# Optimization experiments

Hardware: AMD Instinct MI355X
Metric: run time of the kernel (lower is better)

## Reference

```python
import jax, jax.numpy as jnp
import numpy as np

D_MODEL = 2048
N_HEADS = 16
D_K = D_MODEL // N_HEADS
NB_FEAT = 8  # ceil(ln(2048))
BLOCK_H = 1
BLOCK_W = 1
EPS = 1e-6


def setup_inputs() -> dict:
    key = jax.random.key(0)
    ks = jax.random.split(key, 8)
    B, S = 2, 4096
    q = jax.random.normal(ks[0], (B, S, D_MODEL), dtype=jnp.float32)
    k = jax.random.normal(ks[1], (B, S, D_MODEL), dtype=jnp.float32)
    v = jax.random.normal(ks[2], (B, S, D_MODEL), dtype=jnp.float32)
    # torch Linear weights [out, in]
    w_q = jax.random.normal(ks[3], (D_MODEL, D_MODEL), dtype=jnp.float32) / np.sqrt(D_MODEL)
    w_k = jax.random.normal(ks[4], (D_MODEL, D_MODEL), dtype=jnp.float32) / np.sqrt(D_MODEL)
    w_v = jax.random.normal(ks[5], (D_MODEL, D_MODEL), dtype=jnp.float32) / np.sqrt(D_MODEL)
    w_o = jax.random.normal(ks[6], (D_MODEL, D_MODEL), dtype=jnp.float32) / np.sqrt(D_MODEL)
    omega = jax.random.normal(ks[7], (NB_FEAT, D_K), dtype=jnp.float32) / np.sqrt(D_K)
    return {"q": q, "k": k, "v": v, "w_q": w_q, "w_k": w_k, "w_v": w_v, "w_o": w_o, "omega": omega}


def _kernel(x):
    # kernel_type == 'exp'
    return jnp.exp(-0.5 * x * x)


def reference(q, k, v, w_q, w_k, w_v, w_o, omega):
    B, Sq, D = q.shape
    Sk = k.shape[1]
    # projections (torch Linear: x @ W.T), split heads -> [B, S, H, d_k]
    qh = (q @ w_q.T).reshape(B, Sq, N_HEADS, D_K)
    kh = (k @ w_k.T).reshape(B, Sk, N_HEADS, D_K)
    vh = (v @ w_v.T).reshape(B, Sk, N_HEADS, D_K)
    # random-feature maps -> [B, S, H, nb]
    q_prime = _kernel(jnp.einsum('bshd,nd->bshn', qh, omega))
    k_prime = _kernel(jnp.einsum('bshd,nd->bshn', kh, omega))
    q_prime = q_prime / (q_prime.sum(-1, keepdims=True) + EPS)
    k_prime = k_prime / (k_prime.sum(-1, keepdims=True) + EPS)
    # causal prefix sums along sequence
    K_cum = jnp.cumsum(k_prime, axis=1)                                   # [B,S,H,nb]
    KV_cum = jnp.cumsum(k_prime[..., None] * vh[..., None, :], axis=1)    # [B,S,H,nb,d_k]
    # blockwise causal key selection
    q_idx = jnp.arange(Sq)
    key_idx = jnp.minimum((q_idx // BLOCK_H + 1) * BLOCK_W - 1, Sk - 1)   # [Sq]
    K_sel = K_cum[:, key_idx]    # [B,Sq,H,nb]
    KV_sel = KV_cum[:, key_idx]  # [B,Sq,H,nb,d_k]
    numerator = jnp.einsum('bshn,bshnd->bshd', q_prime, KV_sel)
    denominator = jnp.sum(q_prime * K_sel, axis=-1, keepdims=True)
    out = numerator / (denominator + EPS)
    out = out.reshape(B, Sq, D)
    return out @ w_o.T
```

## Files before the change

### kernel.cpp

```cpp
#include <hip/hip_runtime.h>
#include <hip/hip_bf16.h>
#include <cstdint>

#define B_SZ 2
#define S_LEN 4096
#define R_TOT 8192
#define DM 2048
#define NH 16
#define DK 128
#define NFEAT 8
#define CHUNK 128
#define NCHUNK 32
#define KSPL 256
#define NSPL 8
#define EPSF 1e-6f

typedef short bf16x8_t __attribute__((ext_vector_type(8)));
typedef float f32x4_t __attribute__((ext_vector_type(4)));

__device__ __forceinline__ ushort f2bf(float f) {
  uint32_t u = __float_as_uint(f);
  u += 0x7FFF + ((u >> 16) & 1);
  return (ushort)(u >> 16);
}
__device__ __forceinline__ float bf2f(ushort u) {
  return __uint_as_float(((uint32_t)u) << 16);
}

__global__ __launch_bounds__(256) void prep_kernel(const float* __restrict__ w_v,
                                                   const float* __restrict__ w_o,
                                                   const float* __restrict__ w_q,
                                                   const float* __restrict__ w_k,
                                                   const float* __restrict__ omega,
                                                   ushort* __restrict__ wvb,
                                                   ushort* __restrict__ wob,
                                                   ushort* __restrict__ oqb,
                                                   ushort* __restrict__ okb) {
  const int bid = blockIdx.x;
  if (bid < 8192) {
    const float* src = (bid >= 4096) ? w_o : w_v;
    ushort* dst = (bid >= 4096) ? wob : wvb;
    const int i = (bid & 4095) * 256 + threadIdx.x;
    float4 f = reinterpret_cast<const float4*>(src)[i];
    ushort4 o;
    o.x = f2bf(f.x); o.y = f2bf(f.y); o.z = f2bf(f.z); o.w = f2bf(f.w);
    reinterpret_cast<ushort4*>(dst)[i] = o;
  } else {
    __shared__ float som[NFEAT * DK];
    const int fb = bid - 8192;
    const int z = fb >> 7, h = (fb >> 3) & 15, jb = fb & 7;
    const float* W = z ? w_k : w_q;
    ushort* O = z ? okb : oqb;
    const int j = jb * 256 + threadIdx.x;
    for (int i = threadIdx.x; i < NFEAT * DK; i += 256) som[i] = omega[i];
    __syncthreads();
    float acc[NFEAT] = {0.f, 0.f, 0.f, 0.f, 0.f, 0.f, 0.f, 0.f};
    for (int d = 0; d < DK; d++) {
      const float w = W[(size_t)(h * DK + d) * DM + j];
#pragma unroll
      for (int n = 0; n < NFEAT; n++) acc[n] += w * som[n * DK + d];
    }
#pragma unroll
    for (int n = 0; n < NFEAT; n++) O[(size_t)(h * NFEAT + n) * DM + j] = f2bf(acc[n]);
  }
}

#define MFMA_BLK(mb, A0_, A1_, A2_, A3_, B0_, B1_, B2_, B3_)                                  \
  acc[mb + 0][0] = __builtin_amdgcn_mfma_f32_16x16x32_bf16(A0_, B0_, acc[mb + 0][0], 0, 0, 0); \
  acc[mb + 1][0] = __builtin_amdgcn_mfma_f32_16x16x32_bf16(A1_, B0_, acc[mb + 1][0], 0, 0, 0); \
  acc[mb + 2][0] = __builtin_amdgcn_mfma_f32_16x16x32_bf16(A2_, B0_, acc[mb + 2][0], 0, 0, 0); \
  acc[mb + 3][0] = __builtin_amdgcn_mfma_f32_16x16x32_bf16(A3_, B0_, acc[mb + 3][0], 0, 0, 0); \
  acc[mb + 0][1] = __builtin_amdgcn_mfma_f32_16x16x32_bf16(A0_, B1_, acc[mb + 0][1], 0, 0, 0); \
  acc[mb + 1][1] = __builtin_amdgcn_mfma_f32_16x16x32_bf16(A1_, B1_, acc[mb + 1][1], 0, 0, 0); \
  acc[mb + 2][1] = __builtin_amdgcn_mfma_f32_16x16x32_bf16(A2_, B1_, acc[mb + 2][1], 0, 0, 0); \
  acc[mb + 3][1] = __builtin_amdgcn_mfma_f32_16x16x32_bf16(A3_, B1_, acc[mb + 3][1], 0, 0, 0); \
  acc[mb + 0][2] = __builtin_amdgcn_mfma_f32_16x16x32_bf16(A0_, B2_, acc[mb + 0][2], 0, 0, 0); \
  acc[mb + 1][2] = __builtin_amdgcn_mfma_f32_16x16x32_bf16(A1_, B2_, acc[mb + 1][2], 0, 0, 0); \
  acc[mb + 2][2] = __builtin_amdgcn_mfma_f32_16x16x32_bf16(A2_, B2_, acc[mb + 2][2], 0, 0, 0); \
  acc[mb + 3][2] = __builtin_amdgcn_mfma_f32_16x16x32_bf16(A3_, B2_, acc[mb + 3][2], 0, 0, 0); \
  acc[mb + 0][3] = __builtin_amdgcn_mfma_f32_16x16x32_bf16(A0_, B3_, acc[mb + 0][3], 0, 0, 0); \
  acc[mb + 1][3] = __builtin_amdgcn_mfma_f32_16x16x32_bf16(A1_, B3_, acc[mb + 1][3], 0, 0, 0); \
  acc[mb + 2][3] = __builtin_amdgcn_mfma_f32_16x16x32_bf16(A2_, B3_, acc[mb + 2][3], 0, 0, 0); \
  acc[mb + 3][3] = __builtin_amdgcn_mfma_f32_16x16x32_bf16(A3_, B3_, acc[mb + 3][3], 0, 0, 0);

template<int BF16OUT>
__global__ __launch_bounds__(512, 1) void gemm256(const ushort* __restrict__ A,
                                                  const ushort* __restrict__ Bm,
                                                  void* __restrict__ Cv,
                                                  int M, int N, int K) {
  __shared__ ushort lds[8 * 8192];
  const int tid = threadIdx.x;
  const int wave = tid >> 6, lane = tid & 63;
  const int wm = wave >> 2, wn = wave & 3;
  const int NKT = K >> 6;

  const int nb = N >> 8;
  const int cpx = gridDim.x >> 3;
  const int swz = (blockIdx.x & 7) * cpx + (blockIdx.x >> 3);
  const int bx = swz % nb, by = swz / nb;
  const int m0 = by * 256, n0 = bx * 256;

  auto stage = [&](int bufi, int ab, int kh, int kt, const ushort* G, int r0) {
    ushort* Lr = lds + (((bufi << 1) | ab) << 1 | kh) * 8192;
#pragma unroll
    for (int j = 0; j < 2; j++) {
      const int c = j * 512 + wave * 64 + lane;
      const int row = c >> 2, slot = c & 3;
      const int ss = slot ^ ((row >> 1) & 3);
      const ushort* g = G + (size_t)(r0 + row) * K + kt * 64 + kh * 32 + ss * 8;
      __builtin_amdgcn_global_load_lds(
          (const __attribute__((address_space(1))) void*)g,
          (__attribute__((address_space(3))) void*)(Lr + (j * 512 + wave * 64) * 8), 16, 0, 0);
    }
  };
  auto rdA = [&](int bufi, int kh, int m) -> bf16x8_t {
    const int row = wm * 128 + m * 16 + (lane & 15);
    const int slot = (lane >> 4) ^ ((row >> 1) & 3);
    return *reinterpret_cast<const bf16x8_t*>(lds + ((bufi << 2) | kh) * 8192 + row * 32 + slot * 8);
  };
  auto rdB = [&](int bufi, int kh, int nf) -> bf16x8_t {
    const int row = wn * 64 + nf * 16 + (lane & 15);
    const int slot = (lane >> 4) ^ ((row >> 1) & 3);
    return *reinterpret_cast<const bf16x8_t*>(lds + (((bufi << 1) | 1) << 1 | kh) * 8192 + row * 32 + slot * 8);
  };

  f32x4_t acc[8][4];
#pragma unroll
  for (int m = 0; m < 8; m++)
#pragma unroll
    for (int nf = 0; nf < 4; nf++) acc[m][nf] = (f32x4_t){0.f, 0.f, 0.f, 0.f};

  stage(0, 0, 0, 0, A, m0);  stage(0, 1, 0, 0, Bm, n0);
  stage(0, 0, 1, 0, A, m0);  stage(0, 1, 1, 0, Bm, n0);
  stage(1, 0, 0, 1, A, m0);  stage(1, 1, 0, 1, Bm, n0);
  asm volatile("s_waitcnt vmcnt(8)" ::: "memory");
  __builtin_amdgcn_s_barrier();
  __builtin_amdgcn_sched_barrier(0);

  bf16x8_t pA0 = rdA(0, 0, 0), pA1 = rdA(0, 0, 1), pA2 = rdA(0, 0, 2), pA3 = rdA(0, 0, 3);
  bf16x8_t B00 = rdB(0, 0, 0), B01 = rdB(0, 0, 1), B02 = rdB(0, 0, 2), B03 = rdB(0, 0, 3);
  bf16x8_t qA0, qA1, qA2, qA3, B10, B11, B12, B13;

  for (int t = 0; t < NKT; t++) {
    const int buf = t & 1;
    const int t1 = (t + 1 < NKT) ? t + 1 : NKT - 1;
    const int t2 = (t + 2 < NKT) ? t + 2 : NKT - 1;

    qA0 = rdA(buf, 0, 4); qA1 = rdA(buf, 0, 5); qA2 = rdA(buf, 0, 6); qA3 = rdA(buf, 0, 7);
    stage(buf ^ 1, 0, 1, t1, A, m0);
    __builtin_amdgcn_s_setprio(1);
    MFMA_BLK(0, pA0, pA1, pA2, pA3, B00, B01, B02, B03)
    __builtin_amdgcn_s_setprio(0);
    asm volatile("s_waitcnt vmcnt(6)" ::: "memory");
    __builtin_amdgcn_s_barrier();
    __builtin_amdgcn_sched_barrier(0);

    pA0 = rdA(buf, 1, 0); pA1 = rdA(buf, 1, 1); pA2 = rdA(buf, 1, 2); pA3 = rdA(buf, 1, 3);
    B10 = rdB(buf, 1, 0); B11 = rdB(buf, 1, 1); B12 = rdB(buf, 1, 2); B13 = rdB(buf, 1, 3);
    stage(buf ^ 1, 1, 1, t1, Bm, n0);
    __builtin_amdgcn_s_setprio(1);
    MFMA_BLK(4, qA0, qA1, qA2, qA3, B00, B01, B02, B03)
    __builtin_amdgcn_s_setprio(0);
    __builtin_amdgcn_s_barrier();
    __builtin_amdgcn_sched_barrier(0);

    qA0 = rdA(buf, 1, 4); qA1 = rdA(buf, 1, 5); qA2 = rdA(buf, 1, 6); qA3 = rdA(buf, 1, 7);
    stage(buf, 0, 0, t2, A, m0);
    __builtin_amdgcn_s_setprio(1);
    MFMA_BLK(0, pA0, pA1, pA2, pA3, B10, B11, B12, B13)
    __builtin_amdgcn_s_setprio(0);
    asm volatile("s_waitcnt vmcnt(6)" ::: "memory");
    __builtin_amdgcn_s_barrier();
    __builtin_amdgcn_sched_barrier(0);

    pA0 = rdA(buf ^ 1, 0, 0); pA1 = rdA(buf ^ 1, 0, 1); pA2 = rdA(buf ^ 1, 0, 2); pA3 = rdA(buf ^ 1, 0, 3);
    B00 = rdB(buf ^ 1, 0, 0); B01 = rdB(buf ^ 1, 0, 1); B02 = rdB(buf ^ 1, 0, 2); B03 = rdB(buf ^ 1, 0, 3);
    stage(buf, 1, 0, t2, Bm, n0);
    __builtin_amdgcn_s_setprio(1);
    MFMA_BLK(4, qA0, qA1, qA2, qA3, B10, B11, B12, B13)
    __builtin_amdgcn_s_setprio(0);
    __builtin_amdgcn_s_barrier();
    __builtin_amdgcn_sched_barrier(0);
  }
  asm volatile("s_waitcnt vmcnt(0)" ::: "memory");

#pragma unroll
  for (int m = 0; m < 8; m++) {
    const int rb = m0 + wm * 128 + m * 16 + (lane >> 4) * 4;
#pragma unroll
    for (int nf = 0; nf < 4; nf++) {
      const int col = n0 + wn * 64 + nf * 16 + (lane & 15);
#pragma unroll
      for (int r = 0; r < 4; r++) {
        const float val = acc[m][nf][r];
        if (BF16OUT)
          ((ushort*)Cv)[(size_t)(rb + r) * N + col] = f2bf(val);
        else
          ((float*)Cv)[(size_t)(rb + r) * N + col] = val;
      }
    }
  }
}

__global__ __launch_bounds__(256) void gemm_thin2(const float* __restrict__ qin,
                                                  const float* __restrict__ kin,
                                                  const float* __restrict__ vin,
                                                  const ushort* __restrict__ oqb,
                                                  const ushort* __restrict__ okb,
                                                  ushort* __restrict__ P,
                                                  ushort* __restrict__ xb) {
  __shared__ ushort lds_a[128 * 32];
  __shared__ ushort lds_b[128 * 32];
  const int which = blockIdx.z;
  const float* A = which ? kin : qin;
  const ushort* Bm = which ? okb : oqb;
  const int t = threadIdx.x;
  const int wave = t >> 6, lane = t & 63;
  const int spl = blockIdx.x;
  const int m0 = blockIdx.y * 128;
  const int kb = spl * KSPL;
  const int wm = wave >> 1, wn = wave & 1;
  const int NIT = KSPL / 32;

  const int fbid = (blockIdx.z * gridDim.y + blockIdx.y) * gridDim.x + blockIdx.x;
  const float4* v4 = reinterpret_cast<const float4*>(vin);
  ushort4* x4 = reinterpret_cast<ushort4*>(xb);
  const int vbase = fbid * 4096;

  f32x4_t acc[4][4];
#pragma unroll
  for (int i = 0; i < 4; i++)
#pragma unroll
    for (int j = 0; j < 4; j++) acc[i][j] = (f32x4_t){0.f, 0.f, 0.f, 0.f};

  const int srow = lane >> 2;
  const int skoff = (lane & 3) * 8;
  const int ar0 = t >> 2, ar1 = 64 + (t >> 2), aslot = t & 3;

  const float4* ga0 = reinterpret_cast<const float4*>(A + (size_t)(m0 + ar0) * DM + kb + aslot * 8);
  const float4* ga1 = reinterpret_cast<const float4*>(A + (size_t)(m0 + ar1) * DM + kb + aslot * 8);
  float4 aP0 = ga0[0], aP1 = ga0[1], aP2 = ga1[0], aP3 = ga1[1];
  float4 va = v4[vbase + t], vb = v4[vbase + 256 + t];

  for (int it = 0; it < NIT; ++it) {
    const int k0 = kb + it * 32;
    {
      ushort4 oa, ob;
      oa.x = f2bf(va.x); oa.y = f2bf(va.y); oa.z = f2bf(va.z); oa.w = f2bf(va.w);
      ob.x = f2bf(vb.x); ob.y = f2bf(vb.y); ob.z = f2bf(vb.z); ob.w = f2bf(vb.w);
      x4[vbase + it * 512 + t] = oa;
      x4[vbase + it * 512 + 256 + t] = ob;
    }
    {
      union { ushort u[8]; bf16x8_t v; } p0, p1;
      p0.u[0] = f2bf(aP0.x); p0.u[1] = f2bf(aP0.y); p0.u[2] = f2bf(aP0.z); p0.u[3] = f2bf(aP0.w);
      p0.u[4] = f2bf(aP1.x); p0.u[5] = f2bf(aP1.y); p0.u[6] = f2bf(aP1.z); p0.u[7] = f2bf(aP1.w);
      p1.u[0] = f2bf(aP2.x); p1.u[1] = f2bf(aP2.y); p1.u[2] = f2bf(aP2.z); p1.u[3] = f2bf(aP2.w);
      p1.u[4] = f2bf(aP3.x); p1.u[5] = f2bf(aP3.y); p1.u[6] = f2bf(aP3.z); p1.u[7] = f2bf(aP3.w);
      *reinterpret_cast<bf16x8_t*>(lds_a + ar0 * 32 + aslot * 8) = p0.v;
      *reinterpret_cast<bf16x8_t*>(lds_a + ar1 * 32 + aslot * 8) = p1.v;
    }
#pragma unroll
    for (int i = 0; i < 2; i++) {
      const int rgrp = i * 4 + wave;
      const int row = rgrp * 16 + srow;
      const ushort* gb = Bm + (size_t)row * DM + (k0 + skoff);
      __builtin_amdgcn_global_load_lds(
          (const __attribute__((address_space(1))) void*)gb,
          (__attribute__((address_space(3))) void*)(lds_b + rgrp * 512), 16, 0, 0);
    }
    __builtin_amdgcn_sched_barrier(0);
    if (it + 1 < NIT) {
      const float4* gn0 = reinterpret_cast<const float4*>(A + (size_t)(m0 + ar0) * DM + (k0 + 32) + aslot * 8);
      const float4* gn1 = reinterpret_cast<const float4*>(A + (size_t)(m0 + ar1) * DM + (k0 + 32) + aslot * 8);
      aP0 = gn0[0]; aP1 = gn0[1]; aP2 = gn1[0]; aP3 = gn1[1];
      va = v4[vbase + (it + 1) * 512 + t];
      vb = v4[vbase + (it + 1) * 512 + 256 + t];
      asm volatile("s_waitcnt vmcnt(6) lgkmcnt(0)" ::: "memory");
    } else {
      asm volatile("s_waitcnt vmcnt(0) lgkmcnt(0)" ::: "memory");
    }
    __builtin_amdgcn_s_barrier();
    __builtin_amdgcn_sched_barrier(0);
    bf16x8_t af[4], bfr[4];
#pragma unroll
    for (int i = 0; i < 4; i++) {
      af[i]  = *reinterpret_cast<const bf16x8_t*>(
          lds_a + (wm * 64 + i * 16 + (lane & 15)) * 32 + (lane >> 4) * 8);
      bfr[i] = *reinterpret_cast<const bf16x8_t*>(
          lds_b + (wn * 64 + i * 16 + (lane & 15)) * 32 + (lane >> 4) * 8);
    }
#pragma unroll
    for (int i = 0; i < 4; i++)
#pragma unroll
      for (int j = 0; j < 4; j++)
        acc[i][j] = __builtin_amdgcn_mfma_f32_16x16x32_bf16(af[i], bfr[j], acc[i][j], 0, 0, 0);
    __builtin_amdgcn_s_barrier();
    __builtin_amdgcn_sched_barrier(0);
  }

  ushort* Pp = P + (size_t)which * ((size_t)NSPL * R_TOT * 128) + (size_t)spl * ((size_t)R_TOT * 128);
#pragma unroll
  for (int i = 0; i < 4; i++) {
    const int rb = m0 + wm * 64 + i * 16 + (lane >> 4) * 4;
#pragma unroll
    for (int j = 0; j < 4; j++) {
      const int col = wn * 64 + j * 16 + (lane & 15);
#pragma unroll
      for (int r = 0; r < 4; r++)
        Pp[(size_t)(rb + r) * 128 + col] = f2bf(acc[i][j][r]);
    }
  }
}

__global__ __launch_bounds__(256) void feat2x2(const ushort* __restrict__ P,
                                               float* __restrict__ qf,
                                               float* __restrict__ kf) {
  const int which = blockIdx.y;
  const ushort* Pb = P + (size_t)which * ((size_t)NSPL * R_TOT * 128);
  float* F = which ? kf : qf;
  const int g = blockIdx.x * 256 + threadIdx.x;
  const int row = g >> 4, h = g & 15;
  float x[8] = {0.f, 0.f, 0.f, 0.f, 0.f, 0.f, 0.f, 0.f};
#pragma unroll
  for (int s = 0; s < NSPL; s++) {
    const bf16x8_t u = *reinterpret_cast<const bf16x8_t*>(
        Pb + (size_t)s * ((size_t)R_TOT * 128) + (size_t)row * 128 + h * NFEAT);
#pragma unroll
    for (int n = 0; n < 8; n++) x[n] += bf2f((ushort)u[n]);
  }
  float f[8], sum = 0.f;
#pragma unroll
  for (int n = 0; n < 8; n++) { f[n] = __expf(-0.5f * x[n] * x[n]); sum += f[n]; }
  const float inv = 1.f / (sum + EPSF);
  const int b = row >> 12, sidx = row & 4095;
  float* out = F + ((size_t)(h * 2 + b) * 4096 + sidx) * 8;
  float4 o0 = {f[0] * inv, f[1] * inv, f[2] * inv, f[3] * inv};
  float4 o1 = {f[4] * inv, f[5] * inv, f[6] * inv, f[7] * inv};
  reinterpret_cast<float4*>(out)[0] = o0;
  reinterpret_cast<float4*>(out)[1] = o1;
}

__global__ __launch_bounds__(128) void chunk_sum_kernel(const float* __restrict__ KF,
                                                        const ushort* __restrict__ VH,
                                                        float* __restrict__ CKV,
                                                        float* __restrict__ CK) {
  const int cid = blockIdx.x;
  const int c = cid & 31, bh = cid >> 5, b = bh >> 4, h = bh & 15;
  const int d = threadIdx.x;
  __shared__ float s_kf[CHUNK * 8];
  const size_t fbase = ((size_t)(h * 2 + b) * 4096 + (size_t)c * CHUNK) * 8;
  {
    float4 a0 = *reinterpret_cast<const float4*>(KF + fbase + d * 8);
    float4 a1 = *reinterpret_cast<const float4*>(KF + fbase + d * 8 + 4);
    *reinterpret_cast<float4*>(s_kf + d * 8) = a0;
    *reinterpret_cast<float4*>(s_kf + d * 8 + 4) = a1;
  }
  __syncthreads();
  float kv[8] = {0, 0, 0, 0, 0, 0, 0, 0};
  float ks = 0.f;
  const ushort* vp = VH + ((size_t)b * S_LEN + (size_t)c * CHUNK) * DM + h * DK + d;
  for (int s = 0; s < CHUNK; s++) {
    const float v = bf2f(vp[(size_t)s * DM]);
#pragma unroll
    for (int n = 0; n < 8; n++) kv[n] += s_kf[s * 8 + n] * v;
    ks += s_kf[s * 8 + (d & 7)];
  }
#pragma unroll
  for (int n = 0; n < 8; n++) CKV[((size_t)cid * 8 + n) * 128 + d] = kv[n];
  if (d < 8) CK[cid * 8 + d] = ks;
}

__global__ __launch_bounds__(128) void chunk_scan2(float* __restrict__ CKV,
                                                   float* __restrict__ CK) {
  const int bh = blockIdx.x >> 3, n = blockIdx.x & 7;
  const int d = threadIdx.x;
  float v[NCHUNK];
#pragma unroll
  for (int c = 0; c < NCHUNK; c++)
    v[c] = CKV[((size_t)(bh * NCHUNK + c) * 8 + n) * 128 + d];
  float run = 0.f;
#pragma unroll
  for (int c = 0; c < NCHUNK; c++) {
    const float tv = v[c];
    CKV[((size_t)(bh * NCHUNK + c) * 8 + n) * 128 + d] = run;
    run += tv;
  }
  if (d < 32) {
    const int i = (bh * NCHUNK + d) * 8 + n;
    const float orig = CK[i];
    float inc = orig;
#pragma unroll
    for (int off = 1; off < 32; off <<= 1) {
      const float o = __shfl_up(inc, off, 32);
      if (d >= off) inc += o;
    }
    CK[i] = inc - orig;
  }
}

__global__ __launch_bounds__(128) void attn_scan_kernel(const float* __restrict__ QF,
                                                        const float* __restrict__ KF,
                                                        const ushort* __restrict__ VH,
                                                        const float* __restrict__ CKV,
                                                        const float* __restrict__ CK,
                                                        ushort* __restrict__ AO) {
  const int cid = blockIdx.x;
  const int c = cid & 31, bh = cid >> 5, b = bh >> 4, h = bh & 15;
  const int d = threadIdx.x;
  __shared__ float s_qf[CHUNK * 8];
  __shared__ float s_kf[CHUNK * 8];
  const size_t fbase = ((size_t)(h * 2 + b) * 4096 + (size_t)c * CHUNK) * 8;
  {
    float4 a0 = *reinterpret_cast<const float4*>(QF + fbase + d * 8);
    float4 a1 = *reinterpret_cast<const float4*>(QF + fbase + d * 8 + 4);
    float4 b0 = *reinterpret_cast<const float4*>(KF + fbase + d * 8);
    float4 b1 = *reinterpret_cast<const float4*>(KF + fbase + d * 8 + 4);
    *reinterpret_cast<float4*>(s_qf + d * 8) = a0;
    *reinterpret_cast<float4*>(s_qf + d * 8 + 4) = a1;
    *reinterpret_cast<float4*>(s_kf + d * 8) = b0;
    *reinterpret_cast<float4*>(s_kf + d * 8 + 4) = b1;
  }
  float kv[8], krun[8];
#pragma unroll
  for (int n = 0; n < 8; n++) kv[n] = CKV[((size_t)cid * 8 + n) * 128 + d];
#pragma unroll
  for (int n = 0; n < 8; n++) krun[n] = CK[cid * 8 + n];
  __syncthreads();
  const size_t row0 = (size_t)b * S_LEN + (size_t)c * CHUNK;
  const ushort* vp = VH + row0 * DM + h * DK + d;
  ushort* op = AO + row0 * DM + h * DK + d;
  for (int s = 0; s < CHUNK; s++) {
    const float v = bf2f(vp[(size_t)s * DM]);
    float num = 0.f, den = 0.f;
#pragma unroll
    for (int n = 0; n < 8; n++) {
      const float kf = s_kf[s * 8 + n];
      kv[n] += kf * v;
      krun[n] += kf;
      const float qf = s_qf[s * 8 + n];
      num += qf * kv[n];
      den += qf * krun[n];
    }
    op[(size_t)s * DM] = f2bf(num / (den + EPSF));
  }
}

extern "C" void kernel_launch(void* const* d_in, const int* in_sizes, int n_in,
                              void* d_out, int out_size, void* d_ws, size_t ws_size,
                              hipStream_t stream) {
  const float* q     = (const float*)d_in[0];
  const float* k     = (const float*)d_in[1];
  const float* v     = (const float*)d_in[2];
  const float* w_q   = (const float*)d_in[3];
  const float* w_k   = (const float*)d_in[4];
  const float* w_v   = (const float*)d_in[5];
  const float* w_o   = (const float*)d_in[6];
  const float* omega = (const float*)d_in[7];

  char* ws = (char*)d_ws;
  const size_t DD2 = (size_t)DM * DM * 2;
  const size_t OD2 = (size_t)NH * NFEAT * DM * 2;
  const size_t RD2 = (size_t)R_TOT * DM * 2;
  const size_t X4  = (size_t)R_TOT * NH * NFEAT * 4;

  ushort* wvb = (ushort*)(ws);
  ushort* wob = (ushort*)(ws + DD2);
  ushort* oqb = (ushort*)(ws + 2 * DD2);
  ushort* okb = (ushort*)(ws + 2 * DD2 + OD2);
  ushort* xb  = (ushort*)(ws + 2 * DD2 + 2 * OD2);
  ushort* vhb = (ushort*)(ws + 2 * DD2 + 2 * OD2 + RD2);
  ushort* xp  = (ushort*)(ws + 2 * DD2 + 2 * OD2 + RD2);
  float*  qf  = (float*) (ws + 2 * DD2 + 2 * OD2 + 2 * RD2);
  float*  kf  = (float*) (ws + 2 * DD2 + 2 * OD2 + 2 * RD2 + X4);
  float*  ckv = (float*) (ws + 2 * DD2 + 2 * OD2 + 2 * RD2 + 2 * X4);
  float*  ck  = (float*) (ws + 2 * DD2 + 2 * OD2 + 2 * RD2 + 3 * X4);
  ushort* ao  = xb;

  prep_kernel<<<dim3(8448), 256, 0, stream>>>(w_v, w_o, w_q, w_k, omega,
                                              wvb, wob, oqb, okb);

  gemm_thin2<<<dim3(NSPL, R_TOT / 128, 2), 256, 0, stream>>>(q, k, v, oqb, okb, xp, xb);
  feat2x2<<<dim3(R_TOT * NH / 256, 2), 256, 0, stream>>>(xp, qf, kf);

  gemm256<1><<<dim3((R_TOT / 256) * (DM / 256)), 512, 0, stream>>>(xb, wvb, (void*)vhb, R_TOT, DM, DM);

  chunk_sum_kernel<<<dim3(B_SZ * NH * NCHUNK), 128, 0, stream>>>(kf, vhb, ckv, ck);
  chunk_scan2<<<dim3(B_SZ * NH * 8), 128, 0, stream>>>(ckv, ck);
  attn_scan_kernel<<<dim3(B_SZ * NH * NCHUNK), 128, 0, stream>>>(qf, kf, vhb, ckv, ck, ao);

  gemm256<0><<<dim3((R_TOT / 256) * (DM / 256)), 512, 0, stream>>>(ao, wob, d_out, R_TOT, DM, DM);
}
```

Before: 293.1 us.

## Rewrite thin feature projection GEMM as LDS-free per-wave MFMA kernel

Replaces the LDS-staged, double-barriered thin GEMM that projects q/k onto the folded omega weights with a kernel in which each wave owns 16 rows. A fragments are loaded straight from global memory and converted to bf16 in registers, and B fragments are read directly from global or L2. The grid doubles to 64-row blocks, and the fused fp32-to-bf16 conversion of v is reorganised into a straight unrolled loop. This removes LDS traffic and barriers and adds parallelism. In exchange, B is reloaded from cache by every wave, and the global access pattern is less coalesced.

```diff
diff --git a/kernel.cpp b/kernel.cpp
--- a/kernel.cpp
+++ b/kernel.cpp
@@ -202,114 +202,65 @@
   }
 }
 
-__global__ __launch_bounds__(256) void gemm_thin2(const float* __restrict__ qin,
-                                                  const float* __restrict__ kin,
-                                                  const float* __restrict__ vin,
-                                                  const ushort* __restrict__ oqb,
-                                                  const ushort* __restrict__ okb,
-                                                  ushort* __restrict__ P,
-                                                  ushort* __restrict__ xb) {
-  __shared__ ushort lds_a[128 * 32];
-  __shared__ ushort lds_b[128 * 32];
+__global__ __launch_bounds__(256) void featproj(const float* __restrict__ qin,
+                                                const float* __restrict__ kin,
+                                                const float* __restrict__ vin,
+                                                const ushort* __restrict__ oqb,
+                                                const ushort* __restrict__ okb,
+                                                ushort* __restrict__ P,
+                                                ushort* __restrict__ xb) {
   const int which = blockIdx.z;
   const float* A = which ? kin : qin;
   const ushort* Bm = which ? okb : oqb;
   const int t = threadIdx.x;
   const int wave = t >> 6, lane = t & 63;
+  const int l15 = lane & 15, lk = lane >> 4;
   const int spl = blockIdx.x;
-  const int m0 = blockIdx.y * 128;
+  const int row0 = blockIdx.y * 64 + wave * 16;
   const int kb = spl * KSPL;
-  const int wm = wave >> 1, wn = wave & 1;
-  const int NIT = KSPL / 32;
 
   const int fbid = (blockIdx.z * gridDim.y + blockIdx.y) * gridDim.x + blockIdx.x;
   const float4* v4 = reinterpret_cast<const float4*>(vin);
   ushort4* x4 = reinterpret_cast<ushort4*>(xb);
-  const int vbase = fbid * 4096;
-
-  f32x4_t acc[4][4];
-#pragma unroll
-  for (int i = 0; i < 4; i++)
-#pragma unroll
-    for (int j = 0; j < 4; j++) acc[i][j] = (f32x4_t){0.f, 0.f, 0.f, 0.f};
-
-  const int srow = lane >> 2;
-  const int skoff = (lane & 3) * 8;
-  const int ar0 = t >> 2, ar1 = 64 + (t >> 2), aslot = t & 3;
-
-  const float4* ga0 = reinterpret_cast<const float4*>(A + (size_t)(m0 + ar0) * DM + kb + aslot * 8);
-  const float4* ga1 = reinterpret_cast<const float4*>(A + (size_t)(m0 + ar1) * DM + kb + aslot * 8);
-  float4 aP0 = ga0[0], aP1 = ga0[1], aP2 = ga1[0], aP3 = ga1[1];
-  float4 va = v4[vbase + t], vb = v4[vbase + 256 + t];
-
-  for (int it = 0; it < NIT; ++it) {
-    const int k0 = kb + it * 32;
-    {
-      ushort4 oa, ob;
-      oa.x = f2bf(va.x); oa.y = f2bf(va.y); oa.z = f2bf(va.z); oa.w = f2bf(va.w);
-      ob.x = f2bf(vb.x); ob.y = f2bf(vb.y); ob.z = f2bf(vb.z); ob.w = f2bf(vb.w);
-      x4[vbase + it * 512 + t] = oa;
-      x4[vbase + it * 512 + 256 + t] = ob;
-    }
-    {
-      union { ushort u[8]; bf16x8_t v; } p0, p1;
-      p0.u[0] = f2bf(aP0.x); p0.u[1] = f2bf(aP0.y); p0.u[2] = f2bf(aP0.z); p0.u[3] = f2bf(aP0.w);
-      p0.u[4] = f2bf(aP1.x); p0.u[5] = f2bf(aP1.y); p0.u[6] = f2bf(aP1.z); p0.u[7] = f2bf(aP1.w);
-      p1.u[0] = f2bf(aP2.x); p1.u[1] = f2bf(aP2.y); p1.u[2] = f2bf(aP2.z); p1.u[3] = f2bf(aP2.w);
-      p1.u[4] = f2bf(aP3.x); p1.u[5] = f2bf(aP3.y); p1.u[6] = f2bf(aP3.z); p1.u[7] = f2bf(aP3.w);
-      *reinterpret_cast<bf16x8_t*>(lds_a + ar0 * 32 + aslot * 8) = p0.v;
-      *reinterpret_cast<bf16x8_t*>(lds_a + ar1 * 32 + aslot * 8) = p1.v;
-    }
-#pragma unroll
-    for (int i = 0; i < 2; i++) {
-      const int rgrp = i * 4 + wave;
-      const int row = rgrp * 16 + srow;
-      const ushort* gb = Bm + (size_t)row * DM + (k0 + skoff);
-      __builtin_amdgcn_global_load_lds(
-          (const __attribute__((address_space(1))) void*)gb,
-          (__attribute__((address_space(3))) void*)(lds_b + rgrp * 512), 16, 0, 0);
-    }
-    __builtin_amdgcn_sched_barrier(0);
-    if (it + 1 < NIT) {
-      const float4* gn0 = reinterpret_cast<const float4*>(A + (size_t)(m0 + ar0) * DM + (k0 + 32) + aslot * 8);
-      const float4* gn1 = reinterpret_cast<const float4*>(A + (size_t)(m0 + ar1) * DM + (k0 + 32) + aslot * 8);
-      aP0 = gn0[0]; aP1 = gn0[1]; aP2 = gn1[0]; aP3 = gn1[1];
-      va = v4[vbase + (it + 1) * 512 + t];
-      vb = v4[vbase + (it + 1) * 512 + 256 + t];
-      asm volatile("s_waitcnt vmcnt(6) lgkmcnt(0)" ::: "memory");
-    } else {
-      asm volatile("s_waitcnt vmcnt(0) lgkmcnt(0)" ::: "memory");
-    }
-    __builtin_amdgcn_s_barrier();
-    __builtin_amdgcn_sched_barrier(0);
-    bf16x8_t af[4], bfr[4];
-#pragma unroll
-    for (int i = 0; i < 4; i++) {
-      af[i]  = *reinterpret_cast<const bf16x8_t*>(
-          lds_a + (wm * 64 + i * 16 + (lane & 15)) * 32 + (lane >> 4) * 8);
-      bfr[i] = *reinterpret_cast<const bf16x8_t*>(
-          lds_b + (wn * 64 + i * 16 + (lane & 15)) * 32 + (lane >> 4) * 8);
-    }
-#pragma unroll
-    for (int i = 0; i < 4; i++)
-#pragma unroll
-      for (int j = 0; j < 4; j++)
-        acc[i][j] = __builtin_amdgcn_mfma_f32_16x16x32_bf16(af[i], bfr[j], acc[i][j], 0, 0, 0);
-    __builtin_amdgcn_s_barrier();
-    __builtin_amdgcn_sched_barrier(0);
+  const int vbase = fbid * 2048;
+#pragma unroll
+  for (int i = 0; i < 8; i++) {
+    const float4 f = v4[vbase + i * 256 + t];
+    ushort4 o;
+    o.x = f2bf(f.x); o.y = f2bf(f.y); o.z = f2bf(f.z); o.w = f2bf(f.w);
+    x4[vbase + i * 256 + t] = o;
+  }
+
+  f32x4_t acc[8];
+#pragma unroll
+  for (int cf = 0; cf < 8; cf++) acc[cf] = (f32x4_t){0.f, 0.f, 0.f, 0.f};
+
+  const float* arow = A + (size_t)(row0 + l15) * DM + kb + lk * 8;
+
+#pragma unroll
+  for (int kk = 0; kk < 8; kk++) {
+    const float4 a0 = *reinterpret_cast<const float4*>(arow + kk * 32);
+    const float4 a1 = *reinterpret_cast<const float4*>(arow + kk * 32 + 4);
+    union { ushort u[8]; bf16x8_t v; } pa;
+    pa.u[0] = f2bf(a0.x); pa.u[1] = f2bf(a0.y); pa.u[2] = f2bf(a0.z); pa.u[3] = f2bf(a0.w);
+    pa.u[4] = f2bf(a1.x); pa.u[5] = f2bf(a1.y); pa.u[6] = f2bf(a1.z); pa.u[7] = f2bf(a1.w);
+    const bf16x8_t afr = pa.v;
+#pragma unroll
+    for (int cf = 0; cf < 8; cf++) {
+      const bf16x8_t bfr = *reinterpret_cast<const bf16x8_t*>(
+          Bm + (size_t)(cf * 16 + l15) * DM + kb + kk * 32 + lk * 8);
+      acc[cf] = __builtin_amdgcn_mfma_f32_16x16x32_bf16(afr, bfr, acc[cf], 0, 0, 0);
+    }
   }
 
   ushort* Pp = P + (size_t)which * ((size_t)NSPL * R_TOT * 128) + (size_t)spl * ((size_t)R_TOT * 128);
 #pragma unroll
-  for (int i = 0; i < 4; i++) {
-    const int rb = m0 + wm * 64 + i * 16 + (lane >> 4) * 4;
-#pragma unroll
-    for (int j = 0; j < 4; j++) {
-      const int col = wn * 64 + j * 16 + (lane & 15);
-#pragma unroll
-      for (int r = 0; r < 4; r++)
-        Pp[(size_t)(rb + r) * 128 + col] = f2bf(acc[i][j][r]);
-    }
+  for (int cf = 0; cf < 8; cf++) {
+    const int col = cf * 16 + l15;
+    const int rb = row0 + lk * 4;
+#pragma unroll
+    for (int r = 0; r < 4; r++)
+      Pp[(size_t)(rb + r) * 128 + col] = f2bf(acc[cf][r]);
   }
 }
 
@@ -480,7 +431,7 @@
   prep_kernel<<<dim3(8448), 256, 0, stream>>>(w_v, w_o, w_q, w_k, omega,
                                               wvb, wob, oqb, okb);
 
-  gemm_thin2<<<dim3(NSPL, R_TOT / 128, 2), 256, 0, stream>>>(q, k, v, oqb, okb, xp, xb);
+  featproj<<<dim3(NSPL, R_TOT / 64, 2), 256, 0, stream>>>(q, k, v, oqb, okb, xp, xb);
   feat2x2<<<dim3(R_TOT * NH / 256, 2), 256, 0, stream>>>(xp, qf, kf);
 
   gemm256<1><<<dim3((R_TOT / 256) * (DM / 256)), 512, 0, stream>>>(xb, wvb, (void*)vhb, R_TOT, DM, DM);
```

Result: slower. 343.5 us (+17.2%).
